# Optimization experiments

Hardware: AMD Instinct MI355X
Metric: run time of the kernel (lower is better)

The kernel has to match this reference:

```python
import jax, jax.numpy as jnp
import numpy as np

KS = 6        # kernel_size
NUM_FT = 8    # feat_dim
PAD = [(2, 3)]  # torch conv1d padding='same' for even k=6: left=k-1)//2=2, right=3
DECAY = 0.2   # temporal_decay


def _make_temporal_filters(ft, tao):
    # ft, tao: (1, NUM_FT) raw params
    fts = jax.nn.sigmoid(ft).reshape(NUM_FT, 1) * 0.25                      # (F,1)
    taos = jax.nn.sigmoid(tao).reshape(NUM_FT, 1) * (-KS / np.log(DECAY))   # (F,1)
    t = jnp.arange(KS, dtype=jnp.float32)[None, :]                          # (1,K)
    env = jnp.exp(-t / taos)                                                # (F,K)
    phase = 2.0 * jnp.pi * fts * t                                          # (F,K)
    return env * jnp.sin(phase), env * jnp.cos(phase)                       # (F,K) each


def _dwconv_all_filters(x, filt):
    # x: (B,C,N). filt: (F,K). Depthwise conv (groups=C), same F filters for every
    # channel, all F filters in ONE conv via channel-multiplier layout.
    B, C, N = x.shape
    w = jnp.broadcast_to(filt[None, :, None, :], (C, NUM_FT, 1, KS)).reshape(C * NUM_FT, 1, KS)
    y = jax.lax.conv_general_dilated(
        x, w, window_strides=(1,), padding=PAD,
        dimension_numbers=('NCH', 'OIH', 'NCH'), feature_group_count=C)
    return y.reshape(B, C, NUM_FT, N)  # group g outputs are channels [g*F:(g+1)*F]


def setup_inputs() -> dict:
    key = jax.random.key(0)
    k1, k2, k3 = jax.random.split(key, 3)
    B, C, N = 16, 64, 8192
    x_sin = jax.random.normal(k1, (B, C, N), dtype=jnp.float32)
    x_cos = jax.random.normal(k2, (B, C, N), dtype=jnp.float32)
    # ft initialized as inverse_sigmoid(uniform(0.01, 0.99)), tao = arange(F)/2 + 1
    u = jax.random.uniform(k3, (1, NUM_FT), dtype=jnp.float32, minval=0.01, maxval=0.99)
    ft = jnp.log(u / (1.0 - u))
    tao = (jnp.arange(NUM_FT, dtype=jnp.float32) / 2.0 + 1.0)[None, :]
    return {"x_sin": x_sin, "x_cos": x_cos, "ft": ft, "tao": tao}


def reference(x_sin, x_cos, ft, tao):
    t_sin, t_cos = _make_temporal_filters(ft, tao)           # (F,K) each
    g_o = _dwconv_all_filters(x_sin, t_cos) + _dwconv_all_filters(x_cos, t_sin)
    g_e = _dwconv_all_filters(x_sin, t_sin) - _dwconv_all_filters(x_cos, t_cos)
    me = g_o ** 2 + g_e ** 2                                 # (B,C,F,N)
    # original returns a list of F tensors (B,C,N); stack along leading axis
    return jnp.moveaxis(me, 2, 0)                            # (F,B,C,N)
```

## Files before the change

### kernel.cpp

```cpp
#include <hip/hip_runtime.h>
#include <math.h>

#define BB 16
#define CC 64
#define NN 8192
#define FF 8
#define KK 6
#define TILE 1024
#define NT 256

__global__ __launch_bounds__(NT) void temporal_filter_kernel(
    const float* __restrict__ x_sin, const float* __restrict__ x_cos,
    const float* __restrict__ ft, const float* __restrict__ tao,
    float* __restrict__ out) {
  __shared__ __align__(16) float s_sin[TILE + 8];
  __shared__ __align__(16) float s_cos[TILE + 8];
  __shared__ float s_ts[FF * KK];
  __shared__ float s_tc[FF * KK];

  const int tid = threadIdx.x;
  const int n0 = blockIdx.x * TILE;
  const int row = blockIdx.y;

  if (tid < FF * KK) {
    const int f = tid / KK;
    const float k = (float)(tid % KK);
    const float fts = 0.25f / (1.0f + expf(-ft[f]));
    const float taos = 3.72800961f / (1.0f + expf(-tao[f]));
    const float env = expf(-k / taos);
    const float ph = 6.2831853071795865f * fts * k;
    s_ts[tid] = env * sinf(ph);
    s_tc[tid] = env * cosf(ph);
  }

  const float* xs = x_sin + (size_t)row * NN + n0;
  const float* xc = x_cos + (size_t)row * NN + n0;
  *(float4*)&s_sin[4 + tid * 4] = *(const float4*)&xs[tid * 4];
  *(float4*)&s_cos[4 + tid * 4] = *(const float4*)&xc[tid * 4];
  if (tid < 2) {
    const bool ok = (n0 + tid - 2) >= 0;
    s_sin[2 + tid] = ok ? xs[tid - 2] : 0.0f;
    s_cos[2 + tid] = ok ? xc[tid - 2] : 0.0f;
  } else if (tid < 5) {
    const int j = tid - 2;
    const bool ok = (n0 + TILE + j) < NN;
    s_sin[TILE + 4 + j] = ok ? xs[TILE + j] : 0.0f;
    s_cos[TILE + 4 + j] = ok ? xc[TILE + j] : 0.0f;
  }
  __syncthreads();

  float a[12], b[12];
  {
    const float4* s4 = (const float4*)s_sin;
    float4 v0 = s4[tid], v1 = s4[tid + 1], v2 = s4[tid + 2];
    a[0] = v0.x; a[1] = v0.y; a[2]  = v0.z; a[3]  = v0.w;
    a[4] = v1.x; a[5] = v1.y; a[6]  = v1.z; a[7]  = v1.w;
    a[8] = v2.x; a[9] = v2.y; a[10] = v2.z; a[11] = v2.w;
  }
  {
    const float4* s4 = (const float4*)s_cos;
    float4 v0 = s4[tid], v1 = s4[tid + 1], v2 = s4[tid + 2];
    b[0] = v0.x; b[1] = v0.y; b[2]  = v0.z; b[3]  = v0.w;
    b[4] = v1.x; b[5] = v1.y; b[6]  = v1.z; b[7]  = v1.w;
    b[8] = v2.x; b[9] = v2.y; b[10] = v2.z; b[11] = v2.w;
  }

  float* outp = out + (size_t)row * NN + n0 + tid * 4;
#pragma unroll
  for (int f = 0; f < FF; ++f) {
    float r[4];
#pragma unroll
    for (int j = 0; j < 4; ++j) {
      float go = 0.0f, ge = 0.0f;
#pragma unroll
      for (int k = 0; k < KK; ++k) {
        const float ws = s_ts[f * KK + k];
        const float wc = s_tc[f * KK + k];
        const float vs = a[j + k + 2];
        const float vc = b[j + k + 2];
        go = fmaf(vs, wc, go);
        go = fmaf(vc, ws, go);
        ge = fmaf(vs, ws, ge);
        ge = fmaf(-vc, wc, ge);
      }
      r[j] = go * go + ge * ge;
    }
    *(float4*)(outp + (size_t)f * ((size_t)BB * CC * NN)) =
        make_float4(r[0], r[1], r[2], r[3]);
  }
}

extern "C" void kernel_launch(void* const* d_in, const int* in_sizes, int n_in,
                              void* d_out, int out_size, void* d_ws, size_t ws_size,
                              hipStream_t stream) {
  const float* x_sin = (const float*)d_in[0];
  const float* x_cos = (const float*)d_in[1];
  const float* ft    = (const float*)d_in[2];
  const float* tao   = (const float*)d_in[3];
  float* out = (float*)d_out;

  dim3 grid(NN / TILE, BB * CC);
  temporal_filter_kernel<<<grid, NT, 0, stream>>>(x_sin, x_cos, ft, tao, out);
}
```

Before: 322.9 us.

## Precompute filter weights in separate kernel, drop LDS staging, use nontemporal stores

Result: no change. 321.2 us (-0.5%).

```diff
diff --git a/kernel.cpp b/kernel.cpp
--- a/kernel.cpp
+++ b/kernel.cpp
@@ -6,22 +6,16 @@
 #define NN 8192
 #define FF 8
 #define KK 6
-#define TILE 1024
 #define NT 256
+#define PER_T 4
+#define NBLK_X (NN / (NT * PER_T))
 
-__global__ __launch_bounds__(NT) void temporal_filter_kernel(
-    const float* __restrict__ x_sin, const float* __restrict__ x_cos,
-    const float* __restrict__ ft, const float* __restrict__ tao,
-    float* __restrict__ out) {
-  __shared__ __align__(16) float s_sin[TILE + 8];
-  __shared__ __align__(16) float s_cos[TILE + 8];
-  __shared__ float s_ts[FF * KK];
-  __shared__ float s_tc[FF * KK];
+typedef float float4v __attribute__((ext_vector_type(4)));
 
+__global__ void temporal_filter_weights(const float* __restrict__ ft,
+                                        const float* __restrict__ tao,
+                                        float* __restrict__ w) {
   const int tid = threadIdx.x;
-  const int n0 = blockIdx.x * TILE;
-  const int row = blockIdx.y;
-
   if (tid < FF * KK) {
     const int f = tid / KK;
     const float k = (float)(tid % KK);
@@ -29,53 +23,57 @@
     const float taos = 3.72800961f / (1.0f + expf(-tao[f]));
     const float env = expf(-k / taos);
     const float ph = 6.2831853071795865f * fts * k;
-    s_ts[tid] = env * sinf(ph);
-    s_tc[tid] = env * cosf(ph);
+    w[tid] = env * sinf(ph);
+    w[48 + tid] = env * cosf(ph);
+  }
+}
+
+__global__ __launch_bounds__(NT) void temporal_filter_kernel(
+    const float* __restrict__ x_sin, const float* __restrict__ x_cos,
+    const float* __restrict__ wg, float* __restrict__ out) {
+  const int tid = threadIdx.x;
+  const int row = blockIdx.y;
+  const int p = blockIdx.x * (NT * PER_T) + tid * PER_T;
+
+  float wsin[FF * KK], wcos[FF * KK];
+#pragma unroll
+  for (int i = 0; i < FF * KK; ++i) {
+    wsin[i] = wg[i];
+    wcos[i] = wg[48 + i];
   }
 
-  const float* xs = x_sin + (size_t)row * NN + n0;
-  const float* xc = x_cos + (size_t)row * NN + n0;
-  *(float4*)&s_sin[4 + tid * 4] = *(const float4*)&xs[tid * 4];
-  *(float4*)&s_cos[4 + tid * 4] = *(const float4*)&xc[tid * 4];
-  if (tid < 2) {
-    const bool ok = (n0 + tid - 2) >= 0;
-    s_sin[2 + tid] = ok ? xs[tid - 2] : 0.0f;
-    s_cos[2 + tid] = ok ? xc[tid - 2] : 0.0f;
-  } else if (tid < 5) {
-    const int j = tid - 2;
-    const bool ok = (n0 + TILE + j) < NN;
-    s_sin[TILE + 4 + j] = ok ? xs[TILE + j] : 0.0f;
-    s_cos[TILE + 4 + j] = ok ? xc[TILE + j] : 0.0f;
-  }
-  __syncthreads();
+  const float* xs = x_sin + (size_t)row * NN;
+  const float* xc = x_cos + (size_t)row * NN;
 
   float a[12], b[12];
-  {
-    const float4* s4 = (const float4*)s_sin;
-    float4 v0 = s4[tid], v1 = s4[tid + 1], v2 = s4[tid + 2];
-    a[0] = v0.x; a[1] = v0.y; a[2]  = v0.z; a[3]  = v0.w;
-    a[4] = v1.x; a[5] = v1.y; a[6]  = v1.z; a[7]  = v1.w;
-    a[8] = v2.x; a[9] = v2.y; a[10] = v2.z; a[11] = v2.w;
+  float4v va0 = {0.f, 0.f, 0.f, 0.f}, vb0 = va0, va2 = va0, vb2 = va0;
+  if (p != 0) {
+    va0 = *(const float4v*)&xs[p - 4];
+    vb0 = *(const float4v*)&xc[p - 4];
   }
-  {
-    const float4* s4 = (const float4*)s_cos;
-    float4 v0 = s4[tid], v1 = s4[tid + 1], v2 = s4[tid + 2];
-    b[0] = v0.x; b[1] = v0.y; b[2]  = v0.z; b[3]  = v0.w;
-    b[4] = v1.x; b[5] = v1.y; b[6]  = v1.z; b[7]  = v1.w;
-    b[8] = v2.x; b[9] = v2.y; b[10] = v2.z; b[11] = v2.w;
+  float4v va1 = *(const float4v*)&xs[p];
+  float4v vb1 = *(const float4v*)&xc[p];
+  if (p != NN - PER_T) {
+    va2 = *(const float4v*)&xs[p + 4];
+    vb2 = *(const float4v*)&xc[p + 4];
+  }
+#pragma unroll
+  for (int j = 0; j < 4; ++j) {
+    a[j] = va0[j]; a[4 + j] = va1[j]; a[8 + j] = va2[j];
+    b[j] = vb0[j]; b[4 + j] = vb1[j]; b[8 + j] = vb2[j];
   }
 
-  float* outp = out + (size_t)row * NN + n0 + tid * 4;
+  float* outp = out + (size_t)row * NN + p;
 #pragma unroll
   for (int f = 0; f < FF; ++f) {
-    float r[4];
+    float4v r;
 #pragma unroll
     for (int j = 0; j < 4; ++j) {
       float go = 0.0f, ge = 0.0f;
 #pragma unroll
       for (int k = 0; k < KK; ++k) {
-        const float ws = s_ts[f * KK + k];
-        const float wc = s_tc[f * KK + k];
+        const float ws = wsin[f * KK + k];
+        const float wc = wcos[f * KK + k];
         const float vs = a[j + k + 2];
         const float vc = b[j + k + 2];
         go = fmaf(vs, wc, go);
@@ -85,8 +83,8 @@
       }
       r[j] = go * go + ge * ge;
     }
-    *(float4*)(outp + (size_t)f * ((size_t)BB * CC * NN)) =
-        make_float4(r[0], r[1], r[2], r[3]);
+    __builtin_nontemporal_store(
+        r, (float4v*)(outp + (size_t)f * ((size_t)BB * CC * NN)));
   }
 }
 
@@ -98,7 +96,9 @@
   const float* ft    = (const float*)d_in[2];
   const float* tao   = (const float*)d_in[3];
   float* out = (float*)d_out;
+  float* wg  = (float*)d_ws;
 
-  dim3 grid(NN / TILE, BB * CC);
-  temporal_filter_kernel<<<grid, NT, 0, stream>>>(x_sin, x_cos, ft, tao, out);
+  temporal_filter_weights<<<dim3(1), 64, 0, stream>>>(ft, tao, wg);
+  dim3 grid(NBLK_X, BB * CC);
+  temporal_filter_kernel<<<grid, NT, 0, stream>>>(x_sin, x_cos, wg, out);
 }
```
